# Optimization experiments

Measured on AMD Instinct MI355X. Metric: run time of the kernel, lower is better.

The kernel has to match this reference:

```python
import jax, jax.numpy as jnp
import numpy as np

H = 8  # num_heads (init kwarg)

def setup_inputs() -> dict:
    key = jax.random.key(0)
    k1, k2, k3, k4 = jax.random.split(key, 4)
    B, S, E = 4, 2048, 512
    x = jax.random.normal(k1, (B, S, E), dtype=jnp.float32)
    # 'normal' keras initializer ~ N(0, 0.05)
    Wq = jax.random.normal(k2, (E, E), dtype=jnp.float32) * 0.05
    Wk = jax.random.normal(k3, (E, E), dtype=jnp.float32) * 0.05
    Wv = jax.random.normal(k4, (E, E), dtype=jnp.float32) * 0.05
    return {"x": x, "Wq": Wq, "Wk": Wk, "Wv": Wv}

def _split_heads(t):
    # [B,S,E] -> [H,B,S,E/H]; matches tf.stack(tf.split(t, H, axis=2))
    B, S, E = t.shape
    return t.reshape(B, S, H, E // H).transpose(2, 0, 1, 3)

def reference(x, Wq, Wk, Wv):
    B, S, E = x.shape
    q = _split_heads(jnp.einsum('bse,ef->bsf', x, Wq))  # [H,B,S,dh]
    k = _split_heads(jnp.einsum('bse,ef->bsf', x, Wk))
    v = _split_heads(jnp.einsum('bse,ef->bsf', x, Wv))
    # NOTE: original has NO 1/sqrt(d) scaling
    scores = jnp.einsum('hbqd,hbkd->hbqk', q, k)         # [H,B,S,S]
    attn = jax.nn.softmax(scores, axis=-1)
    effect = jnp.einsum('hbqk,hbkd->hbqd', attn, v)      # [H,B,S,dh]
    # tf.concat(tf.split(effect, H), axis=-1) + squeeze == merge heads on last dim
    out = effect.transpose(1, 2, 0, 3).reshape(B, S, E)  # [B,S,E]
    return (out, x)
```

## Files before the change

### kernel.cpp

```cpp
#include <hip/hip_runtime.h>

typedef _Float16 f16x8 __attribute__((ext_vector_type(8)));
typedef float f32x4 __attribute__((ext_vector_type(4)));
typedef float f32x16 __attribute__((ext_vector_type(16)));

#define GF(r) ((((r)&3)) ^ (((r)>>2)&3))
#define LOG2E 1.44269504088896f

#define GLD16(gp, lp) __builtin_amdgcn_global_load_lds( \
    (const __attribute__((address_space(1))) void*)(gp), \
    (__attribute__((address_space(3))) void*)(lp), 16, 0, 0)

__global__ void cvt_x_kernel(const float4* __restrict__ x4, f16x8* __restrict__ xh,
                             float4* __restrict__ xc, int n8) {
    int i = blockIdx.x * 256 + threadIdx.x;
    if (i >= n8) return;
    float4 a = x4[2 * i], b = x4[2 * i + 1];
    xc[2 * i] = a;
    xc[2 * i + 1] = b;
    f16x8 h;
    h[0] = (_Float16)a.x; h[1] = (_Float16)a.y; h[2] = (_Float16)a.z; h[3] = (_Float16)a.w;
    h[4] = (_Float16)b.x; h[5] = (_Float16)b.y; h[6] = (_Float16)b.z; h[7] = (_Float16)b.w;
    xh[i] = h;
}

__global__ void cvt_w_kernel(const float* __restrict__ Wq, const float* __restrict__ Wk,
                             const float* __restrict__ Wv, _Float16* __restrict__ wt) {
    int j = blockIdx.x * 256 + threadIdx.x;
    if (j >= 786432) return;
    int mat = j >> 18;
    int r = (j >> 9) & 511;
    int n = j & 511;
    const float* W = (mat == 0) ? Wq : ((mat == 1) ? Wk : Wv);
    float v = W[r * 512 + n];
    wt[(size_t)mat * 262144 + (size_t)n * 512 + r] = (_Float16)v;
}

__global__ __launch_bounds__(256, 2) void gemm_qkv(
    const _Float16* __restrict__ xh, const _Float16* __restrict__ wt,
    _Float16* __restrict__ qh, _Float16* __restrict__ kh, _Float16* __restrict__ vt) {
    __shared__ _Float16 lA[128 * 32];
    __shared__ _Float16 lB[128 * 32];
    const int mat = blockIdx.y;
    const _Float16* wp = wt + (size_t)mat * 262144;
    const int mtile = blockIdx.x >> 2, ntile = blockIdx.x & 3;
    const int tid = threadIdx.x, lane = tid & 63;
    const int g = lane >> 4, c = lane & 15;
    const int wid = tid >> 6, wm = wid >> 1, wn = wid & 1;

    f32x4 acc[4][4];
#pragma unroll
    for (int i = 0; i < 4; ++i)
#pragma unroll
        for (int j = 0; j < 4; ++j) acc[i][j] = (f32x4){0.f, 0.f, 0.f, 0.f};

    const int row0 = tid >> 2, p0 = tid & 3;

    for (int ks = 0; ks < 16; ++ks) {
        __syncthreads();
        {
            int r = row0, pp = p0 ^ GF(r);
            GLD16(xh + (size_t)(mtile * 128 + r) * 512 + ks * 32 + pp * 8, &lA[tid * 8]);
            GLD16(wp + (size_t)(ntile * 128 + r) * 512 + ks * 32 + pp * 8, &lB[tid * 8]);
            r = 64 + row0; pp = p0 ^ GF(r);
            GLD16(xh + (size_t)(mtile * 128 + r) * 512 + ks * 32 + pp * 8, &lA[(256 + tid) * 8]);
            GLD16(wp + (size_t)(ntile * 128 + r) * 512 + ks * 32 + pp * 8, &lB[(256 + tid) * 8]);
        }
        __syncthreads();
        f16x8 af[4], bf[4];
#pragma unroll
        for (int i = 0; i < 4; ++i) {
            int ra = wm * 64 + i * 16 + c;
            af[i] = *(const f16x8*)&lA[ra * 32 + ((g ^ GF(ra)) * 8)];
            int rb = wn * 64 + i * 16 + c;
            bf[i] = *(const f16x8*)&lB[rb * 32 + ((g ^ GF(rb)) * 8)];
        }
#pragma unroll
        for (int mi = 0; mi < 4; ++mi)
#pragma unroll
            for (int ni = 0; ni < 4; ++ni)
                acc[mi][ni] = __builtin_amdgcn_mfma_f32_16x16x32_f16(af[mi], bf[ni], acc[mi][ni], 0, 0, 0);
    }

#pragma unroll
    for (int mi = 0; mi < 4; ++mi)
#pragma unroll
        for (int ni = 0; ni < 4; ++ni)
#pragma unroll
            for (int r = 0; r < 4; ++r) {
                int m = mtile * 128 + wm * 64 + mi * 16 + g * 4 + r;
                int n = ntile * 128 + wn * 64 + ni * 16 + c;
                _Float16 hv = (_Float16)acc[mi][ni][r];
                if (mat == 0) {
                    qh[(size_t)m * 512 + n] = hv;
                } else if (mat == 1) {
                    kh[(size_t)m * 512 + n] = hv;
                } else {
                    int h = n >> 6, d = n & 63, bb = m >> 11, s = m & 2047;
                    vt[(((size_t)h * 4 + bb) * 64 + d) * 2048 + s] = hv;
                }
            }
}

__global__ __launch_bounds__(256, 2) void attn_kernel(
    const _Float16* __restrict__ qh, const _Float16* __restrict__ kh,
    const _Float16* __restrict__ vt, float* __restrict__ out) {
    __shared__ _Float16 lK[2][64 * 64];
    __shared__ _Float16 lV[2][64 * 64];
    __shared__ float eb[4][64 * 33];

    const int bid = blockIdx.x;
    const int xcd = bid & 7, idx = bid >> 3;
    const int hb = xcd * 4 + (idx >> 4);
    const int qblk = idx & 15;
    const int h = hb >> 2, b = hb & 3;
    const int tid = threadIdx.x, lane = tid & 63, wid = tid >> 6;
    const int q = lane & 31, hi = lane >> 5;

    const int qrow0 = qblk * 128 + wid * 32;
    const _Float16* qp = qh + ((size_t)b * 2048 + qrow0) * 512 + h * 64;
    const _Float16* kp = kh + (size_t)b * 2048 * 512 + h * 64;
    const _Float16* vp = vt + (size_t)hb * 64 * 2048;

    const int srow = tid >> 3;
    const int ssw = (tid & 7) ^ (srow & 7);

#define STAGE(buf, kt) do { \
    GLD16(kp + ((size_t)((kt) * 64 + srow) * 512) + ssw * 8, &lK[buf][tid * 8]); \
    GLD16(kp + ((size_t)((kt) * 64 + srow + 32) * 512) + ssw * 8, &lK[buf][(tid + 256) * 8]); \
    GLD16(vp + (size_t)srow * 2048 + (kt) * 64 + ssw * 8, &lV[buf][tid * 8]); \
    GLD16(vp + (size_t)(srow + 32) * 2048 + (kt) * 64 + ssw * 8, &lV[buf][(tid + 256) * 8]); \
} while (0)

    f16x8 aQ[4];
#pragma unroll
    for (int kc = 0; kc < 4; ++kc)
        aQ[kc] = *(const f16x8*)(qp + (size_t)q * 512 + kc * 16 + hi * 8);

    float mrow = -1e30f, lrow = 0.f;
    f32x16 o0, o1;
#pragma unroll
    for (int i = 0; i < 16; ++i) { o0[i] = 0.f; o1[i] = 0.f; }

    STAGE(0, 0);
    __syncthreads();

    for (int kt = 0; kt < 32; ++kt) {
        const int cur = kt & 1;
        if (kt < 31) STAGE(cur ^ 1, kt + 1);

        f32x16 s0, s1;
        __builtin_amdgcn_s_setprio(1);
        {
            f32x16 z0, z1;
#pragma unroll
            for (int i = 0; i < 16; ++i) { z0[i] = 0.f; z1[i] = 0.f; }
            const int r0 = q, r1 = 32 + q, sw = q & 7;
#pragma unroll
            for (int kc = 0; kc < 4; ++kc) {
                f16x8 ak0 = *(const f16x8*)&lK[cur][r0 * 64 + (((2 * kc + hi) ^ sw) * 8)];
                f16x8 ak1 = *(const f16x8*)&lK[cur][r1 * 64 + (((2 * kc + hi) ^ sw) * 8)];
                z0 = __builtin_amdgcn_mfma_f32_32x32x16_f16(ak0, aQ[kc], z0, 0, 0, 0);
                z1 = __builtin_amdgcn_mfma_f32_32x32x16_f16(ak1, aQ[kc], z1, 0, 0, 0);
            }
            s0 = z0; s1 = z1;
        }
        __builtin_amdgcn_s_setprio(0);

        float pm;
        {
            float m0 = fmaxf(fmaxf(s0[0], s0[1]), fmaxf(s0[2], s0[3]));
            float m1 = fmaxf(fmaxf(s0[4], s0[5]), fmaxf(s0[6], s0[7]));
            float m2 = fmaxf(fmaxf(s0[8], s0[9]), fmaxf(s0[10], s0[11]));
            float m3 = fmaxf(fmaxf(s0[12], s0[13]), fmaxf(s0[14], s0[15]));
            float m4 = fmaxf(fmaxf(s1[0], s1[1]), fmaxf(s1[2], s1[3]));
            float m5 = fmaxf(fmaxf(s1[4], s1[5]), fmaxf(s1[6], s1[7]));
            float m6 = fmaxf(fmaxf(s1[8], s1[9]), fmaxf(s1[10], s1[11]));
            float m7 = fmaxf(fmaxf(s1[12], s1[13]), fmaxf(s1[14], s1[15]));
            pm = fmaxf(fmaxf(fmaxf(m0, m1), fmaxf(m2, m3)),
                       fmaxf(fmaxf(m4, m5), fmaxf(m6, m7)));
        }
        pm = fmaxf(pm, __shfl_xor(pm, 32));
        const float nm = fmaxf(mrow, pm);
        const float nm2 = nm * LOG2E;
        const float e = __builtin_amdgcn_exp2f(mrow * LOG2E - nm2);
        mrow = nm;

        float rs;
        {
            float a0 = 0.f, a1 = 0.f, a2 = 0.f, a3 = 0.f;
#pragma unroll
            for (int i = 0; i < 4; ++i) {
                float p0 = __builtin_amdgcn_exp2f(fmaf(s0[4 * i + 0], LOG2E, -nm2));
                float p1 = __builtin_amdgcn_exp2f(fmaf(s0[4 * i + 1], LOG2E, -nm2));
                float p2 = __builtin_amdgcn_exp2f(fmaf(s0[4 * i + 2], LOG2E, -nm2));
                float p3 = __builtin_amdgcn_exp2f(fmaf(s0[4 * i + 3], LOG2E, -nm2));
                s0[4 * i + 0] = p0; s0[4 * i + 1] = p1; s0[4 * i + 2] = p2; s0[4 * i + 3] = p3;
                a0 += p0; a1 += p1; a2 += p2; a3 += p3;
            }
#pragma unroll
            for (int i = 0; i < 4; ++i) {
                float p0 = __builtin_amdgcn_exp2f(fmaf(s1[4 * i + 0], LOG2E, -nm2));
                float p1 = __builtin_amdgcn_exp2f(fmaf(s1[4 * i + 1], LOG2E, -nm2));
                float p2 = __builtin_amdgcn_exp2f(fmaf(s1[4 * i + 2], LOG2E, -nm2));
                float p3 = __builtin_amdgcn_exp2f(fmaf(s1[4 * i + 3], LOG2E, -nm2));
                s1[4 * i + 0] = p0; s1[4 * i + 1] = p1; s1[4 * i + 2] = p2; s1[4 * i + 3] = p3;
                a0 += p0; a1 += p1; a2 += p2; a3 += p3;
            }
            rs = (a0 + a1) + (a2 + a3);
        }
        rs += __shfl_xor(rs, 32);
        lrow = lrow * e + rs;

        o0 *= e;
        o1 *= e;

        f16x8 pf[4];
#pragma unroll
        for (int kb = 0; kb < 2; ++kb) {
            const f32x16& sv = kb ? s1 : s0;
            unsigned t0 = __builtin_bit_cast(unsigned, __builtin_amdgcn_cvt_pkrtz(sv[0], sv[1]));
            unsigned t1 = __builtin_bit_cast(unsigned, __builtin_amdgcn_cvt_pkrtz(sv[2], sv[3]));
            unsigned t2 = __builtin_bit_cast(unsigned, __builtin_amdgcn_cvt_pkrtz(sv[4], sv[5]));
            unsigned t3 = __builtin_bit_cast(unsigned, __builtin_amdgcn_cvt_pkrtz(sv[6], sv[7]));
            unsigned t4 = __builtin_bit_cast(unsigned, __builtin_amdgcn_cvt_pkrtz(sv[8], sv[9]));
            unsigned t5 = __builtin_bit_cast(unsigned, __builtin_amdgcn_cvt_pkrtz(sv[10], sv[11]));
            unsigned t6 = __builtin_bit_cast(unsigned, __builtin_amdgcn_cvt_pkrtz(sv[12], sv[13]));
            unsigned t7 = __builtin_bit_cast(unsigned, __builtin_amdgcn_cvt_pkrtz(sv[14], sv[15]));
            asm volatile("v_permlane32_swap_b32 %0, %1" : "+v"(t0), "+v"(t2));
            asm volatile("v_permlane32_swap_b32 %0, %1" : "+v"(t1), "+v"(t3));
            asm volatile("v_permlane32_swap_b32 %0, %1" : "+v"(t4), "+v"(t6));
            asm volatile("v_permlane32_swap_b32 %0, %1" : "+v"(t5), "+v"(t7));
            uint4 u0; u0.x = t0; u0.y = t1; u0.z = t2; u0.w = t3;
            uint4 u1; u1.x = t4; u1.y = t5; u1.z = t6; u1.w = t7;
            pf[2 * kb + 0] = __builtin_bit_cast(f16x8, u0);
            pf[2 * kb + 1] = __builtin_bit_cast(f16x8, u1);
        }

        __builtin_amdgcn_s_setprio(1);
        {
            const int d0 = q, d1 = 32 + q, sw = q & 7;
#pragma unroll
            for (int ck = 0; ck < 4; ++ck) {
                f16x8 av0 = *(const f16x8*)&lV[cur][d0 * 64 + (((2 * ck + hi) ^ sw) * 8)];
                f16x8 av1 = *(const f16x8*)&lV[cur][d1 * 64 + (((2 * ck + hi) ^ sw) * 8)];
                o0 = __builtin_amdgcn_mfma_f32_32x32x16_f16(av0, pf[ck], o0, 0, 0, 0);
                o1 = __builtin_amdgcn_mfma_f32_32x32x16_f16(av1, pf[ck], o1, 0, 0, 0);
            }
        }
        __builtin_amdgcn_s_setprio(0);

        __syncthreads();
    }

    const float inv = 1.0f / lrow;
    float* ebw = eb[wid];
#pragma unroll
    for (int i = 0; i < 16; ++i) {
        int dr = (i & 3) + 8 * (i >> 2) + 4 * hi;
        ebw[dr * 33 + q] = o0[i] * inv;
        ebw[(32 + dr) * 33 + q] = o1[i] * inv;
    }
    __builtin_amdgcn_s_waitcnt(0);
    const int d0c = (lane & 15) * 4;
#pragma unroll
    for (int i = 0; i < 8; ++i) {
        int qr = 4 * i + (lane >> 4);
        float4 v;
        v.x = ebw[(d0c + 0) * 33 + qr];
        v.y = ebw[(d0c + 1) * 33 + qr];
        v.z = ebw[(d0c + 2) * 33 + qr];
        v.w = ebw[(d0c + 3) * 33 + qr];
        *(float4*)(out + ((size_t)b * 2048 + qrow0 + qr) * 512 + h * 64 + d0c) = v;
    }
#undef STAGE
}

extern "C" void kernel_launch(void* const* d_in, const int* in_sizes, int n_in,
                              void* d_out, int out_size, void* d_ws, size_t ws_size,
                              hipStream_t stream) {
    const float* x = (const float*)d_in[0];
    const float* Wq = (const float*)d_in[1];
    const float* Wk = (const float*)d_in[2];
    const float* Wv = (const float*)d_in[3];
    float* out = (float*)d_out;
    float* xcopy = out + 4194304;

    char* ws = (char*)d_ws;
    _Float16* xh = (_Float16*)ws;
    _Float16* wt = (_Float16*)(ws + (size_t)(10u << 20));
    _Float16* qh = (_Float16*)(ws + (size_t)(12u << 20));
    _Float16* kh = (_Float16*)(ws + (size_t)(20u << 20));
    _Float16* vt = (_Float16*)(ws + (size_t)(28u << 20));

    cvt_x_kernel<<<2048, 256, 0, stream>>>((const float4*)x, (f16x8*)xh, (float4*)xcopy, 524288);
    cvt_w_kernel<<<3072, 256, 0, stream>>>(Wq, Wk, Wv, wt);
    gemm_qkv<<<dim3(256, 3), 256, 0, stream>>>(xh, wt, qh, kh, vt);
    attn_kernel<<<512, 256, 0, stream>>>(qh, kh, vt, out);
}
```

Measured before the change: 99.79 us.

## Deepen LDS pipelines to four stages and add lazy softmax rescaling

Both the QKV GEMM and the attention kernel move from single or double buffering to a four-slot LDS ring. Three tiles stay in flight, gated by explicit vmcnt waits and a single barrier per iteration, so global-load latency overlaps the MFMA work. The attention kernel also rescales the running max, sum and output only when a wave's new max exceeds the old one by more than a threshold, which skips most exp and multiply work. Costs: 64KB of LDS per block, which may cut occupancy below the two blocks per CU requested by launch_bounds. The lazy rescale also lets exponent values exceed 1 (up to e^8) before fp16 conversion, a small precision and overflow risk.

```diff
diff --git a/kernel.cpp b/kernel.cpp
--- a/kernel.cpp
+++ b/kernel.cpp
@@ -39,8 +39,7 @@
 __global__ __launch_bounds__(256, 2) void gemm_qkv(
     const _Float16* __restrict__ xh, const _Float16* __restrict__ wt,
     _Float16* __restrict__ qh, _Float16* __restrict__ kh, _Float16* __restrict__ vt) {
-    __shared__ _Float16 lA[128 * 32];
-    __shared__ _Float16 lB[128 * 32];
+    __shared__ __align__(16) char gsm[65536];
     const int mat = blockIdx.y;
     const _Float16* wp = wt + (size_t)mat * 262144;
     const int mtile = blockIdx.x >> 2, ntile = blockIdx.x & 3;
@@ -56,31 +55,55 @@
 
     const int row0 = tid >> 2, p0 = tid & 3;
 
-    for (int ks = 0; ks < 16; ++ks) {
-        __syncthreads();
-        {
-            int r = row0, pp = p0 ^ GF(r);
-            GLD16(xh + (size_t)(mtile * 128 + r) * 512 + ks * 32 + pp * 8, &lA[tid * 8]);
-            GLD16(wp + (size_t)(ntile * 128 + r) * 512 + ks * 32 + pp * 8, &lB[tid * 8]);
-            r = 64 + row0; pp = p0 ^ GF(r);
-            GLD16(xh + (size_t)(mtile * 128 + r) * 512 + ks * 32 + pp * 8, &lA[(256 + tid) * 8]);
-            GLD16(wp + (size_t)(ntile * 128 + r) * 512 + ks * 32 + pp * 8, &lB[(256 + tid) * 8]);
-        }
-        __syncthreads();
+    auto GSTAGE = [&](int buf, int ks) {
+        _Float16* la_ = (_Float16*)(gsm + buf * 16384);
+        _Float16* lb_ = (_Float16*)(gsm + buf * 16384 + 8192);
+        int r = row0, pp = p0 ^ GF(r);
+        GLD16(xh + (size_t)(mtile * 128 + r) * 512 + ks * 32 + pp * 8, &la_[tid * 8]);
+        GLD16(wp + (size_t)(ntile * 128 + r) * 512 + ks * 32 + pp * 8, &lb_[tid * 8]);
+        r = 64 + row0; pp = p0 ^ GF(r);
+        GLD16(xh + (size_t)(mtile * 128 + r) * 512 + ks * 32 + pp * 8, &la_[(256 + tid) * 8]);
+        GLD16(wp + (size_t)(ntile * 128 + r) * 512 + ks * 32 + pp * 8, &lb_[(256 + tid) * 8]);
+    };
+
+    auto GTILE = [&](int ks) {
+        const _Float16* la = (const _Float16*)(gsm + (ks & 3) * 16384);
+        const _Float16* lb = (const _Float16*)(gsm + (ks & 3) * 16384 + 8192);
         f16x8 af[4], bf[4];
 #pragma unroll
         for (int i = 0; i < 4; ++i) {
             int ra = wm * 64 + i * 16 + c;
-            af[i] = *(const f16x8*)&lA[ra * 32 + ((g ^ GF(ra)) * 8)];
+            af[i] = *(const f16x8*)&la[ra * 32 + ((g ^ GF(ra)) * 8)];
             int rb = wn * 64 + i * 16 + c;
-            bf[i] = *(const f16x8*)&lB[rb * 32 + ((g ^ GF(rb)) * 8)];
-        }
+            bf[i] = *(const f16x8*)&lb[rb * 32 + ((g ^ GF(rb)) * 8)];
+        }
+        __builtin_amdgcn_s_setprio(1);
 #pragma unroll
         for (int mi = 0; mi < 4; ++mi)
 #pragma unroll
             for (int ni = 0; ni < 4; ++ni)
                 acc[mi][ni] = __builtin_amdgcn_mfma_f32_16x16x32_f16(af[mi], bf[ni], acc[mi][ni], 0, 0, 0);
+        __builtin_amdgcn_s_setprio(0);
+    };
+
+    GSTAGE(0, 0); GSTAGE(1, 1); GSTAGE(2, 2);
+#pragma unroll 1
+    for (int ks = 0; ks < 13; ++ks) {
+        asm volatile("s_waitcnt vmcnt(8)" ::: "memory");
+        __builtin_amdgcn_s_barrier();
+        __builtin_amdgcn_sched_barrier(0);
+        GSTAGE((ks + 3) & 3, ks + 3);
+        GTILE(ks);
     }
+    asm volatile("s_waitcnt vmcnt(8)" ::: "memory");
+    __builtin_amdgcn_s_barrier();
+    GTILE(13);
+    asm volatile("s_waitcnt vmcnt(4)" ::: "memory");
+    __builtin_amdgcn_s_barrier();
+    GTILE(14);
+    asm volatile("s_waitcnt vmcnt(0)" ::: "memory");
+    __builtin_amdgcn_s_barrier();
+    GTILE(15);
 
 #pragma unroll
     for (int mi = 0; mi < 4; ++mi)
@@ -105,9 +128,7 @@
 __global__ __launch_bounds__(256, 2) void attn_kernel(
     const _Float16* __restrict__ qh, const _Float16* __restrict__ kh,
     const _Float16* __restrict__ vt, float* __restrict__ out) {
-    __shared__ _Float16 lK[2][64 * 64];
-    __shared__ _Float16 lV[2][64 * 64];
-    __shared__ float eb[4][64 * 33];
+    __shared__ __align__(16) char smem[65536];
 
     const int bid = blockIdx.x;
     const int xcd = bid & 7, idx = bid >> 3;
@@ -125,12 +146,14 @@
     const int srow = tid >> 3;
     const int ssw = (tid & 7) ^ (srow & 7);
 
-#define STAGE(buf, kt) do { \
-    GLD16(kp + ((size_t)((kt) * 64 + srow) * 512) + ssw * 8, &lK[buf][tid * 8]); \
-    GLD16(kp + ((size_t)((kt) * 64 + srow + 32) * 512) + ssw * 8, &lK[buf][(tid + 256) * 8]); \
-    GLD16(vp + (size_t)srow * 2048 + (kt) * 64 + ssw * 8, &lV[buf][tid * 8]); \
-    GLD16(vp + (size_t)(srow + 32) * 2048 + (kt) * 64 + ssw * 8, &lV[buf][(tid + 256) * 8]); \
-} while (0)
+    auto STAGE = [&](int buf, int kt) {
+        _Float16* kb_ = (_Float16*)(smem + buf * 16384);
+        _Float16* vb_ = (_Float16*)(smem + buf * 16384 + 8192);
+        GLD16(kp + ((size_t)(kt * 64 + srow) * 512) + ssw * 8, &kb_[tid * 8]);
+        GLD16(kp + ((size_t)(kt * 64 + srow + 32) * 512) + ssw * 8, &kb_[(tid + 256) * 8]);
+        GLD16(vp + (size_t)srow * 2048 + kt * 64 + ssw * 8, &vb_[tid * 8]);
+        GLD16(vp + (size_t)(srow + 32) * 2048 + kt * 64 + ssw * 8, &vb_[(tid + 256) * 8]);
+    };
 
     f16x8 aQ[4];
 #pragma unroll
@@ -142,12 +165,9 @@
 #pragma unroll
     for (int i = 0; i < 16; ++i) { o0[i] = 0.f; o1[i] = 0.f; }
 
-    STAGE(0, 0);
-    __syncthreads();
-
-    for (int kt = 0; kt < 32; ++kt) {
-        const int cur = kt & 1;
-        if (kt < 31) STAGE(cur ^ 1, kt + 1);
+    auto TILE = [&](int kt) {
+        const _Float16* kb = (const _Float16*)(smem + (kt & 3) * 16384);
+        const _Float16* vb = (const _Float16*)(smem + (kt & 3) * 16384 + 8192);
 
         f32x16 s0, s1;
         __builtin_amdgcn_s_setprio(1);
@@ -158,8 +178,8 @@
             const int r0 = q, r1 = 32 + q, sw = q & 7;
 #pragma unroll
             for (int kc = 0; kc < 4; ++kc) {
-                f16x8 ak0 = *(const f16x8*)&lK[cur][r0 * 64 + (((2 * kc + hi) ^ sw) * 8)];
-                f16x8 ak1 = *(const f16x8*)&lK[cur][r1 * 64 + (((2 * kc + hi) ^ sw) * 8)];
+                f16x8 ak0 = *(const f16x8*)&kb[r0 * 64 + (((2 * kc + hi) ^ sw) * 8)];
+                f16x8 ak1 = *(const f16x8*)&kb[r1 * 64 + (((2 * kc + hi) ^ sw) * 8)];
                 z0 = __builtin_amdgcn_mfma_f32_32x32x16_f16(ak0, aQ[kc], z0, 0, 0, 0);
                 z1 = __builtin_amdgcn_mfma_f32_32x32x16_f16(ak1, aQ[kc], z1, 0, 0, 0);
             }
@@ -181,10 +201,15 @@
                        fmaxf(fmaxf(m4, m5), fmaxf(m6, m7)));
         }
         pm = fmaxf(pm, __shfl_xor(pm, 32));
-        const float nm = fmaxf(mrow, pm);
-        const float nm2 = nm * LOG2E;
-        const float e = __builtin_amdgcn_exp2f(mrow * LOG2E - nm2);
-        mrow = nm;
+        if (__any(pm > mrow + 8.0f)) {
+            const float nm = fmaxf(mrow, pm);
+            const float e = __builtin_amdgcn_exp2f((mrow - nm) * LOG2E);
+            mrow = nm;
+            lrow *= e;
+            o0 *= e;
+            o1 *= e;
+        }
+        const float nm2 = mrow * LOG2E;
 
         float rs;
         {
@@ -210,15 +235,12 @@
             rs = (a0 + a1) + (a2 + a3);
         }
         rs += __shfl_xor(rs, 32);
-        lrow = lrow * e + rs;
-
-        o0 *= e;
-        o1 *= e;
+        lrow += rs;
 
         f16x8 pf[4];
 #pragma unroll
-        for (int kb = 0; kb < 2; ++kb) {
-            const f32x16& sv = kb ? s1 : s0;
+        for (int kb2 = 0; kb2 < 2; ++kb2) {
+            const f32x16& sv = kb2 ? s1 : s0;
             unsigned t0 = __builtin_bit_cast(unsigned, __builtin_amdgcn_cvt_pkrtz(sv[0], sv[1]));
             unsigned t1 = __builtin_bit_cast(unsigned, __builtin_amdgcn_cvt_pkrtz(sv[2], sv[3]));
             unsigned t2 = __builtin_bit_cast(unsigned, __builtin_amdgcn_cvt_pkrtz(sv[4], sv[5]));
@@ -233,8 +255,8 @@
             asm volatile("v_permlane32_swap_b32 %0, %1" : "+v"(t5), "+v"(t7));
             uint4 u0; u0.x = t0; u0.y = t1; u0.z = t2; u0.w = t3;
             uint4 u1; u1.x = t4; u1.y = t5; u1.z = t6; u1.w = t7;
-            pf[2 * kb + 0] = __builtin_bit_cast(f16x8, u0);
-            pf[2 * kb + 1] = __builtin_bit_cast(f16x8, u1);
+            pf[2 * kb2 + 0] = __builtin_bit_cast(f16x8, u0);
+            pf[2 * kb2 + 1] = __builtin_bit_cast(f16x8, u1);
         }
 
         __builtin_amdgcn_s_setprio(1);
@@ -242,19 +264,37 @@
             const int d0 = q, d1 = 32 + q, sw = q & 7;
 #pragma unroll
             for (int ck = 0; ck < 4; ++ck) {
-                f16x8 av0 = *(const f16x8*)&lV[cur][d0 * 64 + (((2 * ck + hi) ^ sw) * 8)];
-                f16x8 av1 = *(const f16x8*)&lV[cur][d1 * 64 + (((2 * ck + hi) ^ sw) * 8)];
+                f16x8 av0 = *(const f16x8*)&vb[d0 * 64 + (((2 * ck + hi) ^ sw) * 8)];
+                f16x8 av1 = *(const f16x8*)&vb[d1 * 64 + (((2 * ck + hi) ^ sw) * 8)];
                 o0 = __builtin_amdgcn_mfma_f32_32x32x16_f16(av0, pf[ck], o0, 0, 0, 0);
                 o1 = __builtin_amdgcn_mfma_f32_32x32x16_f16(av1, pf[ck], o1, 0, 0, 0);
             }
         }
         __builtin_amdgcn_s_setprio(0);
-
-        __syncthreads();
+    };
+
+    STAGE(0, 0); STAGE(1, 1); STAGE(2, 2);
+#pragma unroll 1
+    for (int kt = 0; kt < 29; ++kt) {
+        asm volatile("s_waitcnt vmcnt(8)" ::: "memory");
+        __builtin_amdgcn_s_barrier();
+        __builtin_amdgcn_sched_barrier(0);
+        STAGE((kt + 3) & 3, kt + 3);
+        TILE(kt);
     }
-
+    asm volatile("s_waitcnt vmcnt(8)" ::: "memory");
+    __builtin_amdgcn_s_barrier();
+    TILE(29);
+    asm volatile("s_waitcnt vmcnt(4)" ::: "memory");
+    __builtin_amdgcn_s_barrier();
+    TILE(30);
+    asm volatile("s_waitcnt vmcnt(0)" ::: "memory");
+    __builtin_amdgcn_s_barrier();
+    TILE(31);
+
+    __syncthreads();
     const float inv = 1.0f / lrow;
-    float* ebw = eb[wid];
+    float* ebw = (float*)smem + wid * 2112;
 #pragma unroll
     for (int i = 0; i < 16; ++i) {
         int dr = (i & 3) + 8 * (i >> 2) + 4 * hi;
@@ -273,7 +313,6 @@
         v.w = ebw[(d0c + 3) * 33 + qr];
         *(float4*)(out + ((size_t)b * 2048 + qrow0 + qr) * 512 + h * 64 + d0c) = v;
     }
-#undef STAGE
 }
 
 extern "C" void kernel_launch(void* const* d_in, const int* in_sizes, int n_in,
```

Result: no change. 101.3 us (+1.5%).
